# Performance work log

Measured on AMD Instinct MI355X. Metric: run time of the kernel, lower is better.

Reference implementation:

```python
import jax, jax.numpy as jnp
import numpy as np

N, S_CT, D = 64, 128, 1024
WIN = 5
EPS = 1e-8
STOP = 0.1
MAX_DEPTH = 25


def layer_norm(x, g, b, eps=1e-5):
    mu = jnp.mean(x, axis=-1, keepdims=True)
    var = jnp.var(x, axis=-1, keepdims=True)
    return (x - mu) / jnp.sqrt(var + eps) * g + b


def _augment(sequence, input_mask, START, END):
    n, s, d = sequence.shape
    seq = jnp.concatenate([jnp.broadcast_to(START, (n, 1, d)), sequence], axis=1)
    m = jnp.concatenate([jnp.ones((n, 1, 1), seq.dtype), input_mask], axis=1)
    m_no_end = jnp.concatenate([m, jnp.zeros((n, 1, 1), seq.dtype)], axis=1)
    m_yes_end = jnp.concatenate([jnp.ones((n, 1, 1), seq.dtype), m], axis=1)
    end_mask = m_yes_end - m_no_end  # one-hot at END slot
    seq = jnp.concatenate([seq, jnp.zeros((n, 1, d), seq.dtype)], axis=1)
    seq = end_mask * END + (1.0 - end_mask) * seq
    m_no_start = jnp.concatenate([jnp.zeros((n, 1, 1), seq.dtype), m_yes_end[:, 1:]], axis=1)
    return seq, m_yes_end, end_mask, m_no_start, m_no_end


def _neighbor_probs(exist_probs, mask):
    # exist_probs, mask: (n,s,1). Returns left/right soft-neighbor matrices (n,s,s).
    n, s, _ = mask.shape
    m = jnp.stack([mask[:, ::-1, 0], mask[:, :, 0]], axis=1)            # (n,2,s)
    p = jnp.stack([exist_probs[:, ::-1, 0], exist_probs[:, :, 0]], axis=1)
    tri = jnp.triu(jnp.ones((s, s), mask.dtype), k=1)
    mat = (p * m)[:, :, None, :] * tri                                   # (n,2,s,s)
    cs = jnp.cumsum(mat, axis=-1)
    rem_left = jnp.concatenate([jnp.ones((n, 2, s, 1), mask.dtype), 1.0 - cs[..., :-1]], axis=-1)
    rem_left = jnp.maximum(rem_left, 0.0)
    right = jnp.where(cs > 1.0, rem_left, mat) * m[:, :, None, :]
    left = jnp.flip(right[:, 0], axis=(1, 2))
    return left, right[:, 1]


def crvnn_forward(sequence, input_mask, START, END, W_conv, b_conv, W_scorer, b_scorer,
                  W_init, b_init, W_cell1, b_cell1, W_cell2, b_cell2,
                  ln1_g, ln1_b, ln2_g, ln2_b):
    seq, mask, end_mask, m_no_start, m_no_end = _augment(sequence, input_mask, START, END)
    n, s, d = seq.shape
    last_mask = jnp.concatenate([end_mask[:, 1:], jnp.zeros((n, 1, 1), seq.dtype)], axis=1)
    sel_mask = m_no_start * m_no_end * (1.0 - last_mask)  # start_end_last_mask
    seq = layer_norm((seq * mask) @ W_init + b_init, ln1_g, ln1_b) * mask
    exist = jnp.ones((n, s, 1), seq.dtype) * mask

    def step(carry, _):
        sq, ep, um = carry
        L, R = _neighbor_probs(ep, mask)
        l1 = L @ sq; l2 = L @ l1
        r1 = R @ sq; r2 = R @ r1
        win = jnp.concatenate([l2, l1, sq, r1, r2], axis=-1)  # (n,s,5d) == stacked window flattened
        h = jax.nn.gelu(win @ W_conv + b_conv, approximate=False)
        sc = h @ W_scorer + b_scorer                           # (n,s,1) transition score
        scores = jnp.concatenate([sc, jnp.zeros_like(sc)], axis=-1)
        exp_scores = jnp.exp(scores - jnp.max(scores))
        exp_t = exp_scores[..., 0:1] * sel_mask
        exp_n = exp_scores[..., 1:2]
        # sum_normalize over {transition, no_op}; gate halted samples via um (tp=0 => no-op)
        tp = exp_t / (exp_t + exp_n + 2.0 * EPS) * um[:, None, None]
        # compose(left_child, self)
        cat = jnp.concatenate([l1, sq], axis=-1)
        hid = jax.nn.gelu(cat @ W_cell1 + b_cell1, approximate=False)
        contents = (hid @ W_cell2 + b_cell2).reshape(n, s, 4, d)
        gates = jax.nn.sigmoid(contents[:, :, 0:3, :])
        comp = layer_norm(gates[:, :, 0] * l1 + gates[:, :, 1] * sq + gates[:, :, 2] * contents[:, :, 3, :], ln2_g, ln2_b)
        new_sq = tp * comp + (1.0 - tp) * sq
        new_ep = ep * (1.0 - (R @ tp))  # left neighbor consumed with prob of right neighbor transition
        active = jnp.sum(new_ep * sel_mask, axis=(1, 2))
        new_um = um * (active >= STOP).astype(sq.dtype)
        return (new_sq, new_ep, new_um), None

    steps = min(s - 2, MAX_DEPTH)
    (seq, exist, _), _ = jax.lax.scan(step, (seq, exist, jnp.ones((n,), seq.dtype)), None, length=steps)
    seq = seq * mask
    global_state = jnp.sum(last_mask * seq, axis=1)  # root lands at last content slot
    return seq[:, 1:-1, :], global_state


def setup_inputs():
    key = jax.random.key(0)
    ks = jax.random.split(key, 8)
    sc = 0.02
    f32 = jnp.float32
    return {
        "sequence": jax.random.normal(ks[0], (N, S_CT, D), f32),
        "input_mask": jnp.ones((N, S_CT, 1), f32),
        "START": jax.random.normal(ks[1], (D,), f32),
        "END": jax.random.normal(ks[2], (D,), f32),
        "W_conv": jax.random.normal(ks[3], (WIN * D, D), f32) * sc,
        "b_conv": jnp.zeros((D,), f32),
        "W_scorer": jax.random.normal(ks[4], (D, 1), f32) * sc,
        "b_scorer": jnp.zeros((1,), f32),
        "W_init": jax.random.normal(ks[5], (D, D), f32) * sc,
        "b_init": jnp.zeros((D,), f32),
        "W_cell1": jax.random.normal(ks[6], (2 * D, 4 * D), f32) * sc,
        "b_cell1": jnp.zeros((4 * D,), f32),
        "W_cell2": jax.random.normal(ks[7], (4 * D, 4 * D), f32) * sc,
        "b_cell2": jnp.zeros((4 * D,), f32),
        "ln1_g": jnp.ones((D,), f32), "ln1_b": jnp.zeros((D,), f32),
        "ln2_g": jnp.ones((D,), f32), "ln2_b": jnp.zeros((D,), f32),
    }


def reference(sequence, input_mask, START, END, W_conv, b_conv, W_scorer, b_scorer,
              W_init, b_init, W_cell1, b_cell1, W_cell2, b_cell2,
              ln1_g, ln1_b, ln2_g, ln2_b):
    return crvnn_forward(sequence, input_mask, START, END, W_conv, b_conv, W_scorer, b_scorer,
                         W_init, b_init, W_cell1, b_cell1, W_cell2, b_cell2,
                         ln1_g, ln1_b, ln2_g, ln2_b)
```

## Files before the change

kernel.cpp:

```cpp
#include <hip/hip_runtime.h>
#include <math.h>


#define NB 64
#define SS 130
#define DD 1024
#define MM (NB*SS)
#define LSTR 132
#define CROWS 1664
#define RSC 2048.0f
#define IRS (1.0f/2048.0f)

typedef _Float16 f16x8 __attribute__((ext_vector_type(8)));
typedef _Float16 f16x4 __attribute__((ext_vector_type(4)));
typedef _Float16 f16x2 __attribute__((ext_vector_type(2)));
typedef float f32x4 __attribute__((ext_vector_type(4)));

struct GemmSrcF { const float* a[5]; };
struct GemmSrcP { const _Float16* h[5]; const _Float16* l[5]; };
struct hl2 { _Float16 h, l; };

typedef const __attribute__((address_space(1))) void* gas_ptr;
typedef __attribute__((address_space(3))) void* las_ptr;

__device__ __forceinline__ void gload16(const void* g, void* l){
  __builtin_amdgcn_global_load_lds((gas_ptr)g, (las_ptr)l, 16, 0, 0);
}
__device__ __forceinline__ int sw4(int r){ return (r + (r>>2)) & 3; }

__device__ __forceinline__ float bsum(float v){
  __shared__ float sh[4];
  __syncthreads();
  #pragma unroll
  for (int o=32;o;o>>=1) v += __shfl_down(v,o);
  if ((threadIdx.x & 63)==0) sh[threadIdx.x>>6] = v;
  __syncthreads();
  return sh[0]+sh[1]+sh[2]+sh[3];
}
__device__ __forceinline__ float bmaxr(float v){
  __shared__ float sh[4];
  __syncthreads();
  #pragma unroll
  for (int o=32;o;o>>=1) v = fmaxf(v,__shfl_down(v,o));
  if ((threadIdx.x & 63)==0) sh[threadIdx.x>>6] = v;
  __syncthreads();
  return fmaxf(fmaxf(sh[0],sh[1]),fmaxf(sh[2],sh[3]));
}
__device__ __forceinline__ float gelu_(float x){
  return 0.5f*x*(1.f+erff(x*0.70710678118654752f));
}
__device__ __forceinline__ hl2 enc(float x){
  hl2 r;
  r.h = (_Float16)x;
  r.l = (_Float16)((x - (float)r.h)*RSC);
  return r;
}

__global__ __launch_bounds__(256) void build_masks(
    const float* __restrict__ im, float* __restrict__ mk, float* __restrict__ sel,
    float* __restrict__ lastm, float* __restrict__ endm, float* __restrict__ ep,
    float* __restrict__ um, int* __restrict__ flag){
  int b = blockIdx.x, i = threadIdx.x;
  if (i < SS){
    float mye = (i<=1) ? 1.f : im[b*128 + (i-2)];
    float mne = (i==SS-1) ? 0.f : ((i==0) ? 1.f : im[b*128 + (i-1)]);
    float em  = mye - mne;
    float mns = (i==0) ? 0.f : mye;
    float lm;
    if (i < SS-1){
      int i1 = i+1;
      float mye1 = (i1<=1) ? 1.f : im[b*128 + (i1-2)];
      float mne1 = (i1==SS-1) ? 0.f : im[b*128 + (i1-1)];
      lm = mye1 - mne1;
    } else lm = 0.f;
    float sl = mns * mne * (1.f - lm);
    int idx = b*SS + i;
    mk[idx]=mye; sel[idx]=sl; lastm[idx]=lm; endm[idx]=em; ep[idx]=mye;
  } else if (i == SS) { um[b] = 1.f; }
  else if (i == SS+1 && b==0) { flag[0] = 0; }
}

__global__ __launch_bounds__(256) void build_seq(
    const float* __restrict__ seqin, const float* __restrict__ START,
    const float* __restrict__ END, const float* __restrict__ mk,
    const float* __restrict__ endm, float* __restrict__ out){
  int r = blockIdx.x; int b = r/SS, i = r%SS; int t = threadIdx.x;
  float em = endm[r], m = mk[r];
  #pragma unroll
  for (int q=0;q<4;q++){
    int j = t + q*256;
    float v;
    if (i==0) v = START[j];
    else if (i<=128) v = seqin[((size_t)b*128 + (i-1))*DD + j];
    else v = 0.f;
    v = em*END[j] + (1.f-em)*v;
    out[(size_t)r*DD + j] = v*m;
  }
}

__global__ __launch_bounds__(256) void wtranspose(
    const float* __restrict__ W, _Float16* __restrict__ WTh, _Float16* __restrict__ WTl,
    int K, int N){
  __shared__ float Ts[32][33];
  int k0 = blockIdx.x*32, n0 = blockIdx.y*32;
  int t = threadIdx.x;
  int r = t>>3, c4 = (t&7)*4;
  float4 v = *(const float4*)(W + (size_t)(k0+r)*N + n0 + c4);
  Ts[r][c4]=v.x; Ts[r][c4+1]=v.y; Ts[r][c4+2]=v.z; Ts[r][c4+3]=v.w;
  __syncthreads();
  int n = t>>3, k4 = (t&7)*4;
  f16x4 h, lo;
  #pragma unroll
  for (int i=0;i<4;i++){
    hl2 e = enc(Ts[k4+i][n] * 64.f);
    h[i] = e.h; lo[i] = e.l;
  }
  *(f16x4*)(WTh + (size_t)(n0+n)*K + k0+k4) = h;
  *(f16x4*)(WTl + (size_t)(n0+n)*K + k0+k4) = lo;
}

template<bool PREW>
__global__ __launch_bounds__(256,2) void gemm_mfma(
    GemmSrcP S, long lda,
    const _Float16* __restrict__ WTh, const _Float16* __restrict__ WTl,
    const float* __restrict__ Wf, int Nw,
    const float* __restrict__ bias,
    float* __restrict__ C, _Float16* __restrict__ Ch, _Float16* __restrict__ Cl,
    long ldc, int K, int act,
    const int* __restrict__ flag, float* __restrict__ spart, const float* __restrict__ Ws){
  if (flag[0]) return;
  __shared__ _Float16 Ah[128*32], Al[128*32];
  __shared__ _Float16 Wh[128*32], Wl[128*32];
  const int t = threadIdx.x;
  const int wave = t >> 6, lane = t & 63;
  const int wm = wave >> 1, wn = wave & 1;
  const int l15 = lane & 15, l4 = lane >> 4;
  int lin = blockIdx.y * gridDim.x + blockIdx.x;
  int nwg = gridDim.x * gridDim.y;
  int q = nwg >> 3, r = nwg & 7;
  int xcd = lin & 7, pos = lin >> 3;
  int wg = (xcd < r) ? (xcd*(q+1) + pos) : (r*(q+1) + (xcd - r)*q + pos);
  int MT = gridDim.y;
  int mt = wg % MT, nt = wg / MT;
  const long mb = (long)mt * 128;
  const int  nb = nt * 128;
  f32x4 accH[4][4], accX[4][4];
  #pragma unroll
  for (int i=0;i<4;i++)
    #pragma unroll
    for (int j=0;j<4;j++){ accH[i][j] = (f32x4){0.f,0.f,0.f,0.f}; accX[i][j] = (f32x4){0.f,0.f,0.f,0.f}; }

  for (int kt=0; kt<K; kt+=32){
    #pragma unroll
    for (int p=0;p<2;p++){
      int f = t + 256*p;
      int m = f >> 2;
      int qs = f & 3;
      int qd = qs ^ sw4(m);
      int kg = kt + qd*8;
      const _Float16* sh = S.h[kg >> 10];
      const _Float16* sl = S.l[kg >> 10];
      size_t goff = (size_t)(mb + m)*lda + (kg & 1023);
      int lbase = (wave*64 + 256*p)*8;
      gload16(sh + goff, &Ah[lbase]);
      gload16(sl + goff, &Al[lbase]);
    }
    if constexpr (PREW){
      #pragma unroll
      for (int p=0;p<2;p++){
        int f = t + 256*p;
        int n = f >> 2;
        int qs = f & 3;
        int qd = qs ^ sw4(n);
        size_t goff = (size_t)(nb + n)*K + kt + qd*8;
        int lbase = (wave*64 + 256*p)*8;
        gload16(WTh + goff, &Wh[lbase]);
        gload16(WTl + goff, &Wl[lbase]);
      }
    } else {
      #pragma unroll
      for (int p=0;p<2;p++){
        int u = t + 256*p;
        int kp = u >> 5;
        int c  = u & 31;
        const float* wsrc = Wf + (size_t)(kt + 2*kp)*Nw + nb + c;
        #pragma unroll
        for (int i=0;i<4;i++){
          int n = c + 32*i;
          hl2 e0 = enc(wsrc[32*i] * 64.f);
          hl2 e1 = enc(wsrc[(size_t)Nw + 32*i] * 64.f);
          f16x2 hp; hp[0]=e0.h; hp[1]=e1.h;
          f16x2 lp; lp[0]=e0.l; lp[1]=e1.l;
          int slot = (kp>>2) ^ sw4(n);
          int off = n*32 + slot*8 + 2*(kp&3);
          *(f16x2*)&Wh[off] = hp;
          *(f16x2*)&Wl[off] = lp;
        }
      }
    }
    __syncthreads();
    f16x8 wh[4], wl[4];
    #pragma unroll
    for (int i=0;i<4;i++){
      int rw = wn*64 + i*16 + l15;
      int off = rw*32 + (l4 ^ sw4(rw))*8;
      wh[i] = *(const f16x8*)&Wh[off];
      wl[i] = *(const f16x8*)&Wl[off];
    }
    #pragma unroll
    for (int mi=0;mi<4;mi++){
      int ra = wm*64 + mi*16 + l15;
      int off = ra*32 + (l4 ^ sw4(ra))*8;
      f16x8 ahv = *(const f16x8*)&Ah[off];
      f16x8 alv = *(const f16x8*)&Al[off];
      #pragma unroll
      for (int ni=0;ni<4;ni++){
        accH[mi][ni] = __builtin_amdgcn_mfma_f32_16x16x32_f16(wh[ni], ahv, accH[mi][ni], 0,0,0);
        accX[mi][ni] = __builtin_amdgcn_mfma_f32_16x16x32_f16(wh[ni], alv, accX[mi][ni], 0,0,0);
        accX[mi][ni] = __builtin_amdgcn_mfma_f32_16x16x32_f16(wl[ni], ahv, accX[mi][ni], 0,0,0);
      }
    }
    __syncthreads();
  }

  const float IH = 1.f/64.f, IX = 1.f/131072.f;
  if (act==2){
    #pragma unroll
    for (int mi=0;mi<4;mi++){
      float s = 0.f;
      #pragma unroll
      for (int ni=0;ni<4;ni++){
        int nbase = nb + wn*64 + ni*16 + 4*l4;
        #pragma unroll
        for (int rr=0;rr<4;rr++){
          float v = gelu_(accH[mi][ni][rr]*IH + accX[mi][ni][rr]*IX + bias[nbase+rr]);
          s = fmaf(v, Ws[nbase+rr], s);
        }
      }
      s += __shfl_xor(s, 16);
      s += __shfl_xor(s, 32);
      if (l4==0){
        long m = mb + wm*64 + mi*16 + l15;
        spart[m*16 + nt*2 + wn] = s;
      }
    }
    return;
  }
  #pragma unroll
  for (int mi=0;mi<4;mi++){
    long m = mb + wm*64 + mi*16 + l15;
    #pragma unroll
    for (int ni=0;ni<4;ni++){
      int nbase = nb + wn*64 + ni*16 + 4*l4;
      float v0 = accH[mi][ni][0]*IH + accX[mi][ni][0]*IX + bias[nbase+0];
      float v1 = accH[mi][ni][1]*IH + accX[mi][ni][1]*IX + bias[nbase+1];
      float v2 = accH[mi][ni][2]*IH + accX[mi][ni][2]*IX + bias[nbase+2];
      float v3 = accH[mi][ni][3]*IH + accX[mi][ni][3]*IX + bias[nbase+3];
      if (act==1){
        v0=gelu_(v0); v1=gelu_(v1); v2=gelu_(v2); v3=gelu_(v3);
        hl2 e0=enc(v0), e1=enc(v1), e2=enc(v2), e3=enc(v3);
        f16x4 h4; h4[0]=e0.h; h4[1]=e1.h; h4[2]=e2.h; h4[3]=e3.h;
        f16x4 l4v; l4v[0]=e0.l; l4v[1]=e1.l; l4v[2]=e2.l; l4v[3]=e3.l;
        *(f16x4*)(Ch + m*ldc + nbase) = h4;
        *(f16x4*)(Cl + m*ldc + nbase) = l4v;
      } else {
        float4 v; v.x=v0; v.y=v1; v.z=v2; v.w=v3;
        *(float4*)(C + m*ldc + nbase) = v;
      }
    }
  }
}

__global__ __launch_bounds__(256,2) void gemm_f32(
    GemmSrcF S, long lda, const float* __restrict__ B, const float* __restrict__ bias,
    float* __restrict__ C, long ldc, int N, int K, int act,
    const int* __restrict__ flag){
  if (flag[0]) return;
  __shared__ float Asm[16][132];
  __shared__ float Bsm[16][132];
  float acc[8][8];
  #pragma unroll
  for (int i=0;i<8;i++)
    #pragma unroll
    for (int j=0;j<8;j++) acc[i][j]=0.f;
  const int t = threadIdx.x;
  const int tx = t & 15, ty = t >> 4;
  const long mb = (long)blockIdx.y * 128;
  const int  nb = blockIdx.x * 128;
  for (int kt=0; kt<K; kt+=16){
    #pragma unroll
    for (int ii=0; ii<2; ii++){
      int f  = t + 256*ii;
      int m  = f >> 2;
      int k4 = (f & 3) * 4;
      int kg = kt + k4;
      const float* src = S.a[kg >> 10];
      float4 v = *(const float4*)(src + (mb + m)*lda + (kg & 1023));
      Asm[k4+0][m]=v.x; Asm[k4+1][m]=v.y; Asm[k4+2][m]=v.z; Asm[k4+3][m]=v.w;
    }
    #pragma unroll
    for (int ii=0; ii<2; ii++){
      int f  = t + 256*ii;
      int kk = f >> 5;
      int c4 = (f & 31)*4;
      *(float4*)&Bsm[kk][c4] = *(const float4*)(B + (long)(kt+kk)*N + nb + c4);
    }
    __syncthreads();
    #pragma unroll
    for (int kk=0;kk<16;kk++){
      float av[8], bv[8];
      *(float4*)&av[0] = *(const float4*)&Asm[kk][ty*4];
      *(float4*)&av[4] = *(const float4*)&Asm[kk][64+ty*4];
      *(float4*)&bv[0] = *(const float4*)&Bsm[kk][tx*4];
      *(float4*)&bv[4] = *(const float4*)&Bsm[kk][64+tx*4];
      #pragma unroll
      for (int r=0;r<8;r++)
        #pragma unroll
        for (int c=0;c<8;c++) acc[r][c] = fmaf(av[r],bv[c],acc[r][c]);
    }
    __syncthreads();
  }
  #pragma unroll
  for (int rh=0;rh<2;rh++)
  #pragma unroll
  for (int rr=0;rr<4;rr++){
    long row = mb + rh*64 + ty*4 + rr;
    #pragma unroll
    for (int ch=0;ch<2;ch++){
      int col = nb + ch*64 + tx*4;
      float4 v;
      v.x = acc[rh*4+rr][ch*4+0] + bias[col+0];
      v.y = acc[rh*4+rr][ch*4+1] + bias[col+1];
      v.z = acc[rh*4+rr][ch*4+2] + bias[col+2];
      v.w = acc[rh*4+rr][ch*4+3] + bias[col+3];
      *(float4*)(C + row*ldc + col) = v;
    }
  }
}

__global__ __launch_bounds__(256,2) void bgemm(
    const float* __restrict__ P,
    const _Float16* __restrict__ Xh, const _Float16* __restrict__ Xl,
    _Float16* __restrict__ Yh, _Float16* __restrict__ Yl,
    const int* __restrict__ flag){
  if (flag[0]) return;
  __shared__ float Ps[64][17];
  __shared__ float Xs[16][132];
  const int t = threadIdx.x;
  const int nt = blockIdx.x, mt = blockIdx.y, b = blockIdx.z;
  const int i0 = mt*64;
  const float* Pb = P + (size_t)b*SS*LSTR;
  const _Float16* Xhb = Xh + (size_t)b*SS*DD + nt*128;
  const _Float16* Xlb = Xl + (size_t)b*SS*DD + nt*128;
  _Float16* Yhb = Yh + (size_t)b*SS*DD + nt*128;
  _Float16* Ylb = Yl + (size_t)b*SS*DD + nt*128;
  const int tx = t & 7, ty = t >> 3;
  float acc[2][16];
  #pragma unroll
  for (int r=0;r<2;r++)
    #pragma unroll
    for (int c=0;c<16;c++) acc[r][c]=0.f;
  for (int j0=0;j0<SS;j0+=16){
    { int r = t>>2, c0 = (t&3)*4;
      float4 v = make_float4(0.f,0.f,0.f,0.f);
      if (i0 + r < SS && j0 + c0 < LSTR) v = *(const float4*)(Pb + (size_t)(i0+r)*LSTR + j0 + c0);
      Ps[r][c0]=v.x; Ps[r][c0+1]=v.y; Ps[r][c0+2]=v.z; Ps[r][c0+3]=v.w;
    }
    #pragma unroll
    for (int ii=0;ii<2;ii++){
      int f = t + 256*ii;
      int jj = f>>5, c4 = (f&31)*4;
      float x0=0.f,x1=0.f,x2=0.f,x3=0.f;
      if (j0 + jj < SS){
        f16x4 xh = *(const f16x4*)(Xhb + (size_t)(j0+jj)*DD + c4);
        f16x4 xl = *(const f16x4*)(Xlb + (size_t)(j0+jj)*DD + c4);
        x0 = (float)xh[0] + (float)xl[0]*IRS;
        x1 = (float)xh[1] + (float)xl[1]*IRS;
        x2 = (float)xh[2] + (float)xl[2]*IRS;
        x3 = (float)xh[3] + (float)xl[3]*IRS;
      }
      Xs[jj][c4]=x0; Xs[jj][c4+1]=x1; Xs[jj][c4+2]=x2; Xs[jj][c4+3]=x3;
    }
    __syncthreads();
    #pragma unroll
    for (int jj=0;jj<16;jj++){
      float p0 = Ps[2*ty][jj], p1 = Ps[2*ty+1][jj];
      #pragma unroll
      for (int q=0;q<4;q++){
        float4 xv = *(const float4*)&Xs[jj][tx*4 + 32*q];
        acc[0][q*4+0] = fmaf(p0,xv.x,acc[0][q*4+0]);
        acc[0][q*4+1] = fmaf(p0,xv.y,acc[0][q*4+1]);
        acc[0][q*4+2] = fmaf(p0,xv.z,acc[0][q*4+2]);
        acc[0][q*4+3] = fmaf(p0,xv.w,acc[0][q*4+3]);
        acc[1][q*4+0] = fmaf(p1,xv.x,acc[1][q*4+0]);
        acc[1][q*4+1] = fmaf(p1,xv.y,acc[1][q*4+1]);
        acc[1][q*4+2] = fmaf(p1,xv.z,acc[1][q*4+2]);
        acc[1][q*4+3] = fmaf(p1,xv.w,acc[1][q*4+3]);
      }
    }
    __syncthreads();
  }
  #pragma unroll
  for (int rr=0;rr<2;rr++){
    int row = i0 + 2*ty + rr;
    if (row < SS){
      #pragma unroll
      for (int q=0;q<4;q++){
        hl2 e0 = enc(acc[rr][q*4+0]);
        hl2 e1 = enc(acc[rr][q*4+1]);
        hl2 e2 = enc(acc[rr][q*4+2]);
        hl2 e3 = enc(acc[rr][q*4+3]);
        f16x4 h4; h4[0]=e0.h; h4[1]=e1.h; h4[2]=e2.h; h4[3]=e3.h;
        f16x4 l4v; l4v[0]=e0.l; l4v[1]=e1.l; l4v[2]=e2.l; l4v[3]=e3.l;
        *(f16x4*)(Yhb + (size_t)row*DD + tx*4 + 32*q) = h4;
        *(f16x4*)(Ylb + (size_t)row*DD + tx*4 + 32*q) = l4v;
      }
    }
  }
}

__global__ __launch_bounds__(256) void neighbor_kernel(
    const float* __restrict__ ep, const float* __restrict__ mk,
    float* __restrict__ L, float* __restrict__ R, const int* __restrict__ flag){
  if (flag[0]) return;
  int wave = threadIdx.x >> 6, lane = threadIdx.x & 63;
  int idx = blockIdx.x*4 + wave;
  if (idx >= MM) return;
  int b = idx / SS, i = idx % SS;
  const float* p = ep + b*SS;
  const float* m = mk + b*SS;
  float mR[3], mL[3], mv[3];
  #pragma unroll
  for (int c=0;c<3;c++){
    int j = lane + 64*c;
    float pj = (j<SS)? p[j] : 0.f;
    float mj = (j<SS)? m[j] : 0.f;
    mv[c] = mj;
    float x = pj*mj;
    mR[c] = (j>i)? x : 0.f;
    mL[c] = (j<i)? x : 0.f;
  }
  float csR[3]; float run = 0.f;
  #pragma unroll
  for (int c=0;c<3;c++){
    float s = mR[c];
    #pragma unroll
    for (int o=1;o<64;o<<=1){ float v = __shfl_up(s,o); if (lane>=o) s += v; }
    csR[c] = s + run;
    run += __shfl(s,63);
  }
  float csL[3]; run = 0.f;
  #pragma unroll
  for (int cc=0;cc<3;cc++){
    int c = 2-cc;
    float s = mL[c];
    #pragma unroll
    for (int o=1;o<64;o<<=1){ float v = __shfl_down(s,o); if (lane < 64-o) s += v; }
    csL[c] = s + run;
    run += __shfl(s,0);
  }
  float* Lr = L + (size_t)idx*LSTR;
  float* Rr = R + (size_t)idx*LSTR;
  #pragma unroll
  for (int c=0;c<3;c++){
    int j = lane + 64*c;
    if (j < LSTR){
      float rv = 0.f, lv = 0.f;
      if (j < SS){
        rv = ((csR[c]>1.f) ? fmaxf(1.f-(csR[c]-mR[c]),0.f) : mR[c]) * mv[c];
        lv = ((csL[c]>1.f) ? fmaxf(1.f-(csL[c]-mL[c]),0.f) : mL[c]) * mv[c];
      }
      Rr[j] = rv; Lr[j] = lv;
    }
  }
}

__global__ __launch_bounds__(256) void ln1_kernel(
    const float* __restrict__ xin, const float* __restrict__ g, const float* __restrict__ bb,
    const float* __restrict__ mk, _Float16* __restrict__ sqh, _Float16* __restrict__ sql){
  int r = blockIdx.x, t = threadIdx.x;
  const float* xr = xin + (size_t)r*DD;
  float x[4]; float s=0.f;
  #pragma unroll
  for (int q=0;q<4;q++){ x[q]=xr[t+256*q]; s+=x[q]; }
  float mean = bsum(s)*(1.f/DD);
  float vs=0.f;
  #pragma unroll
  for (int q=0;q<4;q++){ float d=x[q]-mean; vs+=d*d; }
  float var = bsum(vs)*(1.f/DD);
  float inv = 1.f/sqrtf(var+1e-5f);
  float m = mk[r];
  #pragma unroll
  for (int q=0;q<4;q++){
    int j=t+256*q;
    float v = ((x[q]-mean)*inv*g[j]+bb[j])*m;
    hl2 e = enc(v);
    sqh[(size_t)r*DD+j] = e.h; sql[(size_t)r*DD+j] = e.l;
  }
}

__global__ void scorer_final(const float* __restrict__ spart, const float* __restrict__ bs,
                             float* __restrict__ sc, const int* __restrict__ flag){
  if (flag[0]) return;
  int r = blockIdx.x*blockDim.x + threadIdx.x;
  if (r >= MM) return;
  float s = bs[0];
  #pragma unroll
  for (int k=0;k<16;k++) s += spart[(size_t)r*16+k];
  sc[r] = s;
}
__global__ __launch_bounds__(256) void max1(const float* __restrict__ sc, float* __restrict__ part,
                                            const int* __restrict__ flag){
  if (flag[0]) return;
  int idx = blockIdx.x*256 + threadIdx.x;
  float v = -1e30f;
  for (int i = idx; i < MM; i += 64*256) v = fmaxf(v, sc[i]);
  v = bmaxr(v);
  if (threadIdx.x==0) part[blockIdx.x] = v;
}
__global__ __launch_bounds__(64) void max2(const float* __restrict__ part, float* __restrict__ gm,
                                           const int* __restrict__ flag){
  if (flag[0]) return;
  float v = part[threadIdx.x];
  #pragma unroll
  for (int o=32;o;o>>=1) v = fmaxf(v, __shfl_down(v,o));
  if (threadIdx.x==0) gm[0] = fmaxf(v, 0.f);
}
__global__ void tp_kernel(const float* __restrict__ sc, const float* __restrict__ sel,
                          const float* __restrict__ um, const float* __restrict__ gm,
                          float* __restrict__ tp, const int* __restrict__ flag){
  if (flag[0]) return;
  int idx = blockIdx.x*blockDim.x + threadIdx.x;
  if (idx>=MM) return;
  int b = idx / SS;
  float g = gm[0];
  float et = expf(sc[idx]-g)*sel[idx];
  float en = expf(-g);
  tp[idx] = et/(et+en+2e-8f)*um[b];
}

__global__ __launch_bounds__(256) void update_kernel(
    const float* __restrict__ cont,
    const _Float16* __restrict__ l1h, const _Float16* __restrict__ l1l,
    _Float16* __restrict__ sqh, _Float16* __restrict__ sql,
    const float* __restrict__ tp, const float* __restrict__ g, const float* __restrict__ bb,
    const int* __restrict__ flag, long row0){
  if (flag[0]) return;
  long r = row0 + blockIdx.x; int t = threadIdx.x;
  const float* cr = cont + (size_t)blockIdx.x*4096;
  const _Float16* lh = l1h + (size_t)r*DD;
  const _Float16* ll = l1l + (size_t)r*DD;
  _Float16* sh = sqh + (size_t)r*DD;
  _Float16* sl = sql + (size_t)r*DD;
  float x[4], sv[4];
  float s=0.f;
  #pragma unroll
  for (int q=0;q<4;q++){
    int j = t+q*256;
    float c0=cr[j], c1=cr[DD+j], c2=cr[2*DD+j], c3=cr[3*DD+j];
    float g0=1.f/(1.f+expf(-c0));
    float g1=1.f/(1.f+expf(-c1));
    float g2=1.f/(1.f+expf(-c2));
    float lv = (float)lh[j] + (float)ll[j]*IRS;
    float sqv = (float)sh[j] + (float)sl[j]*IRS;
    sv[q]=sqv;
    x[q] = g0*lv + g1*sqv + g2*c3;
    s += x[q];
  }
  float mean = bsum(s)*(1.f/DD);
  float vs=0.f;
  #pragma unroll
  for (int q=0;q<4;q++){ float d=x[q]-mean; vs+=d*d; }
  float var = bsum(vs)*(1.f/DD);
  float inv = 1.f/sqrtf(var+1e-5f);
  float tpv = tp[r];
  #pragma unroll
  for (int q=0;q<4;q++){
    int j=t+q*256;
    float comp = (x[q]-mean)*inv*g[j]+bb[j];
    float out = tpv*comp + (1.f-tpv)*sv[q];
    hl2 e = enc(out);
    sh[j]=e.h; sl[j]=e.l;
  }
}

__global__ __launch_bounds__(256) void ep_update(
    float* __restrict__ ep, const float* __restrict__ R,
    const float* __restrict__ tp, const int* __restrict__ flag){
  if (flag[0]) return;
  int wave = threadIdx.x >> 6, lane = threadIdx.x & 63;
  int idx = blockIdx.x*4 + wave;
  if (idx >= MM) return;
  int b = idx / SS;
  const float* Rr = R + (size_t)idx*LSTR;
  const float* tb = tp + b*SS;
  float d = 0.f;
  #pragma unroll
  for (int c=0;c<3;c++){
    int j = lane + 64*c;
    if (j < SS) d = fmaf(Rr[j], tb[j], d);
  }
  #pragma unroll
  for (int o=32;o;o>>=1) d += __shfl_xor(d,o);
  if (lane==0) ep[idx] *= (1.f - d);
}

__global__ __launch_bounds__(256) void active_um(const float* __restrict__ ep,
                                                 const float* __restrict__ sel,
                                                 float* __restrict__ um,
                                                 const int* __restrict__ flag){
  if (flag[0]) return;
  int b = blockIdx.x, t = threadIdx.x;
  float s = (t<SS) ? ep[b*SS+t]*sel[b*SS+t] : 0.f;
  s = bsum(s);
  if (t==0) um[b] *= (s >= 0.1f) ? 1.f : 0.f;
}
__global__ __launch_bounds__(64) void done_kernel(const float* __restrict__ um, int* __restrict__ flag){
  float v = um[threadIdx.x];
  unsigned long long b = __ballot(v > 0.f);
  if (threadIdx.x==0) flag[0] = (b==0ULL) ? 1 : 0;
}

__global__ __launch_bounds__(256) void output_kernel(
    const _Float16* __restrict__ sqh, const _Float16* __restrict__ sql,
    const float* __restrict__ mk, float* __restrict__ out){
  int r = blockIdx.x; int b = r/SS, i = r%SS;
  if (i<1 || i>128) return;
  float m = mk[r]; int t=threadIdx.x;
  #pragma unroll
  for (int q=0;q<4;q++){
    int j = t+q*256;
    float v = (float)sqh[(size_t)r*DD+j] + (float)sql[(size_t)r*DD+j]*IRS;
    out[((size_t)b*128 + (i-1))*DD + j] = v*m;
  }
}
__global__ __launch_bounds__(256) void gstate_kernel(
    const _Float16* __restrict__ sqh, const _Float16* __restrict__ sql,
    const float* __restrict__ mk, const float* __restrict__ lastm,
    float* __restrict__ outg){
  int b = blockIdx.x; int t=threadIdx.x;
  #pragma unroll
  for (int q=0;q<4;q++){
    int j = t+q*256;
    float acc=0.f;
    for (int i=0;i<SS;i++){
      float w = lastm[b*SS+i]*mk[b*SS+i];
      size_t o = ((size_t)(b*SS+i))*DD + j;
      float v = (float)sqh[o] + (float)sql[o]*IRS;
      acc = fmaf(w, v, acc);
    }
    outg[(size_t)b*DD + j] = acc;
  }
}

extern "C" void kernel_launch(void* const* d_in, const int* in_sizes, int n_in,
                              void* d_out, int out_size, void* d_ws, size_t ws_size,
                              hipStream_t stream) {
  const float* sequence   = (const float*)d_in[0];
  const float* input_mask = (const float*)d_in[1];
  const float* START      = (const float*)d_in[2];
  const float* END        = (const float*)d_in[3];
  const float* W_conv     = (const float*)d_in[4];
  const float* b_conv     = (const float*)d_in[5];
  const float* W_scorer   = (const float*)d_in[6];
  const float* b_scorer   = (const float*)d_in[7];
  const float* W_init     = (const float*)d_in[8];
  const float* b_init     = (const float*)d_in[9];
  const float* W_cell1    = (const float*)d_in[10];
  const float* b_cell1    = (const float*)d_in[11];
  const float* W_cell2    = (const float*)d_in[12];
  const float* b_cell2    = (const float*)d_in[13];
  const float* ln1g       = (const float*)d_in[14];
  const float* ln1b       = (const float*)d_in[15];
  const float* ln2g       = (const float*)d_in[16];
  const float* ln2b       = (const float*)d_in[17];

  float* ws = (float*)d_ws;
  const size_t U = (size_t)MM*DD;
  _Float16* sq_h = (_Float16*)(ws);        _Float16* sq_l = sq_h + U;
  _Float16* l1_h = (_Float16*)(ws + U);    _Float16* l1_l = l1_h + U;
  _Float16* r1_h = (_Float16*)(ws + 2*U);  _Float16* r1_l = r1_h + U;
  _Float16* l2_h = (_Float16*)(ws + 3*U);  _Float16* l2_l = l2_h + U;
  _Float16* r2_h = (_Float16*)(ws + 4*U);  _Float16* r2_l = r2_h + U;
  float* contb = ws + 4*U;
  float* seqtmp  = ws + U;
  float* inittmp = ws + 2*U;
  float* Lm   = ws + 5*U;
  float* Rm   = Lm + (size_t)NB*SS*LSTR;
  float* maskv= Rm + (size_t)NB*SS*LSTR;
  float* sel  = maskv + MM;
  float* lastm= sel + MM;
  float* endm = lastm + MM;
  float* ep   = endm + MM;
  float* scb  = ep + MM;
  float* tpb  = scb + MM;
  float* spart= tpb + MM;
  float* umb  = spart + (size_t)MM*16;
  float* part = umb + NB;
  float* gmx  = part + 64;
  int*   flag = (int*)(gmx + 4);
  size_t used_floats = (size_t)((float*)(flag+4) - ws);
  used_floats = (used_floats + 7) & ~(size_t)7;
  const size_t SC = (size_t)1024*5120, S1 = (size_t)4096*2048, S2 = (size_t)4096*4096;
  _Float16* WT2_h = (_Float16*)(ws + used_floats);
  _Float16* WT2_l = WT2_h + S2;
  _Float16* WT1_h = WT2_l + S2;
  _Float16* WT1_l = WT1_h + S1;
  _Float16* WTc_h = WT1_l + S1;
  _Float16* WTc_l = WTc_h + SC;
  const bool pre2 = ws_size >= (size_t)((char*)(WT2_l + S2) - (char*)d_ws);
  const bool pre1 = ws_size >= (size_t)((char*)(WT1_l + S1) - (char*)d_ws);
  const bool prec = ws_size >= (size_t)((char*)(WTc_l + SC) - (char*)d_ws);

  build_masks<<<NB,256,0,stream>>>(input_mask, maskv, sel, lastm, endm, ep, umb, flag);
  build_seq<<<MM,256,0,stream>>>(sequence, START, END, maskv, endm, seqtmp);
  GemmSrcF si; si.a[0]=seqtmp; si.a[1]=seqtmp; si.a[2]=seqtmp; si.a[3]=seqtmp; si.a[4]=seqtmp;
  gemm_f32<<<dim3(8,65),256,0,stream>>>(si, DD, W_init, b_init, inittmp, DD, DD, DD, 0, flag);
  ln1_kernel<<<MM,256,0,stream>>>(inittmp, ln1g, ln1b, maskv, sq_h, sq_l);

  if (pre2) wtranspose<<<dim3(128,128),256,0,stream>>>(W_cell2, WT2_h, WT2_l, 4096, 4096);
  if (pre1) wtranspose<<<dim3(64,128),256,0,stream>>>(W_cell1, WT1_h, WT1_l, 2048, 4096);
  if (prec) wtranspose<<<dim3(160,32),256,0,stream>>>(W_conv,  WTc_h, WTc_l, 5120, 1024);

  const int NBLK = (MM + 3) / 4;
  for (int it=0; it<25; ++it){
    neighbor_kernel<<<NBLK,256,0,stream>>>(ep, maskv, Lm, Rm, flag);
    bgemm<<<dim3(8,3,NB),256,0,stream>>>(Lm, sq_h, sq_l, l1_h, l1_l, flag);
    bgemm<<<dim3(8,3,NB),256,0,stream>>>(Rm, sq_h, sq_l, r1_h, r1_l, flag);
    bgemm<<<dim3(8,3,NB),256,0,stream>>>(Lm, l1_h, l1_l, l2_h, l2_l, flag);
    bgemm<<<dim3(8,3,NB),256,0,stream>>>(Rm, r1_h, r1_l, r2_h, r2_l, flag);
    GemmSrcP s5;
    s5.h[0]=l2_h; s5.h[1]=l1_h; s5.h[2]=sq_h; s5.h[3]=r1_h; s5.h[4]=r2_h;
    s5.l[0]=l2_l; s5.l[1]=l1_l; s5.l[2]=sq_l; s5.l[3]=r1_l; s5.l[4]=r2_l;
    if (prec)
      gemm_mfma<true ><<<dim3(8,65),256,0,stream>>>(s5, DD, WTc_h, WTc_l, nullptr, 0, b_conv, nullptr, nullptr, nullptr, 0, 5120, 2, flag, spart, W_scorer);
    else
      gemm_mfma<false><<<dim3(8,65),256,0,stream>>>(s5, DD, nullptr, nullptr, W_conv, 1024, b_conv, nullptr, nullptr, nullptr, 0, 5120, 2, flag, spart, W_scorer);
    scorer_final<<<(MM+255)/256,256,0,stream>>>(spart, b_scorer, scb, flag);
    max1<<<64,256,0,stream>>>(scb, part, flag);
    max2<<<1,64,0,stream>>>(part, gmx, flag);
    tp_kernel<<<(MM+255)/256,256,0,stream>>>(scb, sel, umb, gmx, tpb, flag);
    for (int c=0;c<5;c++){
      long row0 = (long)c*CROWS;
      GemmSrcP s2;
      s2.h[0]=l1_h+row0*DD; s2.h[1]=sq_h+row0*DD; s2.h[2]=s2.h[1]; s2.h[3]=s2.h[1]; s2.h[4]=s2.h[1];
      s2.l[0]=l1_l+row0*DD; s2.l[1]=sq_l+row0*DD; s2.l[2]=s2.l[1]; s2.l[3]=s2.l[1]; s2.l[4]=s2.l[1];
      GemmSrcP s3;
      s3.h[0]=l2_h; s3.h[1]=l2_h+DD; s3.h[2]=l2_h+2*DD; s3.h[3]=l2_h+3*DD; s3.h[4]=l2_h;
      s3.l[0]=l2_l; s3.l[1]=l2_l+DD; s3.l[2]=l2_l+2*DD; s3.l[3]=l2_l+3*DD; s3.l[4]=l2_l;
      if (pre1)
        gemm_mfma<true ><<<dim3(32,13),256,0,stream>>>(s2, DD,   WT1_h, WT1_l, nullptr, 0, b_cell1, nullptr, l2_h, l2_l, 4096, 2048, 1, flag, nullptr, nullptr);
      else
        gemm_mfma<false><<<dim3(32,13),256,0,stream>>>(s2, DD,   nullptr, nullptr, W_cell1, 4096, b_cell1, nullptr, l2_h, l2_l, 4096, 2048, 1, flag, nullptr, nullptr);
      if (pre2)
        gemm_mfma<true ><<<dim3(32,13),256,0,stream>>>(s3, 4096, WT2_h, WT2_l, nullptr, 0, b_cell2, contb, nullptr, nullptr, 4096, 4096, 0, flag, nullptr, nullptr);
      else
        gemm_mfma<false><<<dim3(32,13),256,0,stream>>>(s3, 4096, nullptr, nullptr, W_cell2, 4096, b_cell2, contb, nullptr, nullptr, 4096, 4096, 0, flag, nullptr, nullptr);
      update_kernel<<<CROWS,256,0,stream>>>(contb, l1_h, l1_l, sq_h, sq_l, tpb, ln2g, ln2b, flag, row0);
    }
    ep_update<<<NBLK,256,0,stream>>>(ep, Rm, tpb, flag);
    active_um<<<NB,256,0,stream>>>(ep, sel, umb, flag);
    done_kernel<<<1,64,0,stream>>>(umb, flag);
  }

  float* out = (float*)d_out;
  output_kernel<<<MM,256,0,stream>>>(sq_h, sq_l, maskv, out);
  gstate_kernel<<<NB,256,0,stream>>>(sq_h, sq_l, maskv, lastm, out + (size_t)NB*128*DD);
}
```

Measured before the change: 62.08 ms.

## Double-buffer GEMM LDS tiles to overlap global loads with MFMA compute

Converts the split-fp16 MFMA GEMM mainloop to a two-stage ping-pong LDS buffer. The next K-tile is issued with direct-to-LDS loads while the current tile is computed, with explicit vmcnt waits and raw s_barrier calls. This hides global load latency but doubles LDS use to 64KB per block, which may reduce occupancy under launch_bounds(256,2). The hand-counted vmcnt waits and the unchanged LDS writes on the non-PREW path risk ordering subtleties.

```diff
diff --git a/kernel.cpp b/kernel.cpp
--- a/kernel.cpp
+++ b/kernel.cpp
@@ -129,8 +129,8 @@
     long ldc, int K, int act,
     const int* __restrict__ flag, float* __restrict__ spart, const float* __restrict__ Ws){
   if (flag[0]) return;
-  __shared__ _Float16 Ah[128*32], Al[128*32];
-  __shared__ _Float16 Wh[128*32], Wl[128*32];
+  __shared__ _Float16 Ah[2][128*32], Al[2][128*32];
+  __shared__ _Float16 Wh[2][128*32], Wl[2][128*32];
   const int t = threadIdx.x;
   const int wave = t >> 6, lane = t & 63;
   const int wm = wave >> 1, wn = wave & 1;
@@ -150,34 +150,8 @@
     #pragma unroll
     for (int j=0;j<4;j++){ accH[i][j] = (f32x4){0.f,0.f,0.f,0.f}; accX[i][j] = (f32x4){0.f,0.f,0.f,0.f}; }
 
-  for (int kt=0; kt<K; kt+=32){
-    #pragma unroll
-    for (int p=0;p<2;p++){
-      int f = t + 256*p;
-      int m = f >> 2;
-      int qs = f & 3;
-      int qd = qs ^ sw4(m);
-      int kg = kt + qd*8;
-      const _Float16* sh = S.h[kg >> 10];
-      const _Float16* sl = S.l[kg >> 10];
-      size_t goff = (size_t)(mb + m)*lda + (kg & 1023);
-      int lbase = (wave*64 + 256*p)*8;
-      gload16(sh + goff, &Ah[lbase]);
-      gload16(sl + goff, &Al[lbase]);
-    }
-    if constexpr (PREW){
-      #pragma unroll
-      for (int p=0;p<2;p++){
-        int f = t + 256*p;
-        int n = f >> 2;
-        int qs = f & 3;
-        int qd = qs ^ sw4(n);
-        size_t goff = (size_t)(nb + n)*K + kt + qd*8;
-        int lbase = (wave*64 + 256*p)*8;
-        gload16(WTh + goff, &Wh[lbase]);
-        gload16(WTl + goff, &Wl[lbase]);
-      }
-    } else {
+  auto stage = [&](int bf, int kt){
+    if constexpr (!PREW){
       #pragma unroll
       for (int p=0;p<2;p++){
         int u = t + 256*p;
@@ -193,26 +167,65 @@
           f16x2 lp; lp[0]=e0.l; lp[1]=e1.l;
           int slot = (kp>>2) ^ sw4(n);
           int off = n*32 + slot*8 + 2*(kp&3);
-          *(f16x2*)&Wh[off] = hp;
-          *(f16x2*)&Wl[off] = lp;
+          *(f16x2*)&Wh[bf][off] = hp;
+          *(f16x2*)&Wl[bf][off] = lp;
         }
       }
-    }
-    __syncthreads();
+    } else {
+      #pragma unroll
+      for (int p=0;p<2;p++){
+        int f = t + 256*p;
+        int n = f >> 2;
+        int qd = (f & 3) ^ sw4(n);
+        size_t goff = (size_t)(nb + n)*K + kt + qd*8;
+        int lbase = (wave*64 + 256*p)*8;
+        gload16(WTh + goff, &Wh[bf][lbase]);
+        gload16(WTl + goff, &Wl[bf][lbase]);
+      }
+    }
+    #pragma unroll
+    for (int p=0;p<2;p++){
+      int f = t + 256*p;
+      int m = f >> 2;
+      int qd = (f & 3) ^ sw4(m);
+      int kg = kt + qd*8;
+      const _Float16* shp = S.h[kg >> 10];
+      const _Float16* slp = S.l[kg >> 10];
+      size_t goff = (size_t)(mb + m)*lda + (kg & 1023);
+      int lbase = (wave*64 + 256*p)*8;
+      gload16(shp + goff, &Ah[bf][lbase]);
+      gload16(slp + goff, &Al[bf][lbase]);
+    }
+  };
+
+  const int ntile = K >> 5;
+  int cur = 0;
+  stage(0, 0);
+  asm volatile("s_waitcnt vmcnt(0) lgkmcnt(0)" ::: "memory");
+  __builtin_amdgcn_s_barrier();
+  for (int tt=0; tt<ntile; ++tt){
+    if (tt+1 < ntile){
+      stage(cur^1, (tt+1)<<5);
+      if constexpr (PREW) asm volatile("s_waitcnt vmcnt(8)" ::: "memory");
+      else                asm volatile("s_waitcnt vmcnt(4)" ::: "memory");
+    } else {
+      asm volatile("s_waitcnt vmcnt(0)" ::: "memory");
+    }
+    __builtin_amdgcn_s_barrier();
     f16x8 wh[4], wl[4];
     #pragma unroll
     for (int i=0;i<4;i++){
       int rw = wn*64 + i*16 + l15;
       int off = rw*32 + (l4 ^ sw4(rw))*8;
-      wh[i] = *(const f16x8*)&Wh[off];
-      wl[i] = *(const f16x8*)&Wl[off];
+      wh[i] = *(const f16x8*)&Wh[cur][off];
+      wl[i] = *(const f16x8*)&Wl[cur][off];
     }
     #pragma unroll
     for (int mi=0;mi<4;mi++){
       int ra = wm*64 + mi*16 + l15;
       int off = ra*32 + (l4 ^ sw4(ra))*8;
-      f16x8 ahv = *(const f16x8*)&Ah[off];
-      f16x8 alv = *(const f16x8*)&Al[off];
+      f16x8 ahv = *(const f16x8*)&Ah[cur][off];
+      f16x8 alv = *(const f16x8*)&Al[cur][off];
       #pragma unroll
       for (int ni=0;ni<4;ni++){
         accH[mi][ni] = __builtin_amdgcn_mfma_f32_16x16x32_f16(wh[ni], ahv, accH[mi][ni], 0,0,0);
@@ -220,7 +233,8 @@
         accX[mi][ni] = __builtin_amdgcn_mfma_f32_16x16x32_f16(wl[ni], ahv, accX[mi][ni], 0,0,0);
       }
     }
-    __syncthreads();
+    __builtin_amdgcn_s_barrier();
+    cur ^= 1;
   }
 
   const float IH = 1.f/64.f, IX = 1.f/131072.f;
```

Result: no change. 62.86 ms (+1.3%).
